# Performance work log

Measured on AMD Instinct MI355X. Metric: run time of the kernel, lower is better.

Reference implementation:

```python
import jax, jax.numpy as jnp
import numpy as np

B, N, C, H = 8, 4096, 1024, 16
D = C // H
SCALE = D ** -0.5

def setup_inputs() -> dict:
    key = jax.random.key(0)
    ks = jax.random.split(key, 6)
    s = C ** -0.5
    return {
        "fea": jax.random.normal(ks[0], (B, N, C), jnp.float32),
        "embedding": jax.random.normal(ks[1], (B, 1, C), jnp.float32),
        "Wq": jax.random.normal(ks[2], (C, C), jnp.float32) * s,
        "Wk": jax.random.normal(ks[3], (C, C), jnp.float32) * s,
        "Wv": jax.random.normal(ks[4], (C, C), jnp.float32) * s,
        "Wp": jax.random.normal(ks[5], (C, C), jnp.float32) * s,
        "bp": jnp.zeros((C,), jnp.float32),
    }

def reference(fea, embedding, Wq, Wk, Wv, Wp, bp):
    # q: [B,N,H,D]; k,v: [B,H,D] (kv seq len is 1)
    q = (fea @ Wq.T).reshape(B, N, H, D)
    k = (embedding @ Wk.T).reshape(B, H, D)
    v = (embedding @ Wv.T).reshape(B, H, D)
    # attn scores [B,N,H]: single-token key -> per-head dot product
    attn = jax.nn.sigmoid(jnp.einsum("bnhd,bhd->bnh", q, k) * SCALE)
    # broadcast-weight v over sequence: [B,N,H,D] -> [B,N,C]
    feat = (attn[..., None] * v[:, None, :, :]).reshape(B, N, C)
    feat = feat @ Wp.T + bp
    return feat + fea
```

## Files before the change

kernel.cpp:

```cpp
#include <hip/hip_runtime.h>
#include <hip/hip_bf16.h>
#include <stdint.h>

#define B 8
#define N 4096
#define C 1024
#define H 16
#define D 64

static __device__ __forceinline__ float bf_lo(uint32_t u) {
    union { uint32_t i; float f; } c; c.i = u << 16; return c.f;
}
static __device__ __forceinline__ float bf_hi(uint32_t u) {
    union { uint32_t i; float f; } c; c.i = u & 0xffff0000u; return c.f;
}

__global__ __launch_bounds__(256, 2)
void kv_kernel(const float* __restrict__ emb,
               const float* __restrict__ Wk,
               const float* __restrict__ Wv,
               float* __restrict__ kbuf,
               float* __restrict__ vbuf) {
    int wave = (blockIdx.x * blockDim.x + threadIdx.x) >> 6;
    int lane = threadIdx.x & 63;
    int r = wave;
    const float* Wrow = (r < C) ? (Wk + (size_t)r * C) : (Wv + (size_t)(r - C) * C);
    float4 w4[4];
#pragma unroll
    for (int j = 0; j < 4; ++j) w4[j] = *(const float4*)(Wrow + (lane + 64 * j) * 4);
    float acc[B];
#pragma unroll
    for (int b = 0; b < B; ++b) {
        const float* e = emb + (size_t)b * C;
        float a = 0.f;
#pragma unroll
        for (int j = 0; j < 4; ++j) {
            float4 e4 = *(const float4*)(e + (lane + 64 * j) * 4);
            a += w4[j].x * e4.x + w4[j].y * e4.y + w4[j].z * e4.z + w4[j].w * e4.w;
        }
        acc[b] = a;
    }
#pragma unroll
    for (int off = 32; off; off >>= 1)
#pragma unroll
        for (int b = 0; b < B; ++b) acc[b] += __shfl_xor(acc[b], off, 64);
    if (lane == 0) {
        float* dst = (r < C) ? (kbuf + r) : (vbuf + (r - C));
#pragma unroll
        for (int b = 0; b < B; ++b) dst[b * C] = acc[b];
    }
}

__global__ __launch_bounds__(256, 2)
void wu_kernel(const float* __restrict__ Wq,
               const float* __restrict__ Wp,
               const float* __restrict__ kbuf,
               const float* __restrict__ vbuf,
               __hip_bfloat16* __restrict__ wbuf,
               __hip_bfloat16* __restrict__ ubuf) {
    int id = blockIdx.x;
    int which = id & 1; id >>= 1;
    int h = id % H;
    int b = id / H;
    int t = threadIdx.x;
    if (which == 0) {
        const float* kk = kbuf + (size_t)(b * H + h) * D;
        int c = t * 4;
        float4 acc = {0.f, 0.f, 0.f, 0.f};
#pragma unroll 8
        for (int d = 0; d < D; ++d) {
            float kvs = kk[d];
            float4 w4 = *(const float4*)(Wq + (size_t)(h * D + d) * C + c);
            acc.x += kvs * w4.x; acc.y += kvs * w4.y;
            acc.z += kvs * w4.z; acc.w += kvs * w4.w;
        }
        __hip_bfloat16* o = wbuf + (size_t)(b * H + h) * C + c;
        o[0] = __float2bfloat16(acc.x); o[1] = __float2bfloat16(acc.y);
        o[2] = __float2bfloat16(acc.z); o[3] = __float2bfloat16(acc.w);
    } else {
        const int q = t & 3;
        const float* vv = vbuf + (size_t)(b * H + h) * D + q * 16;
        float4 v4[4];
#pragma unroll
        for (int m = 0; m < 4; ++m) v4[m] = *(const float4*)(vv + m * 4);
#pragma unroll
        for (int p = 0; p < 16; ++p) {
            int cp = p * 64 + (t >> 2);
            const float* wp = Wp + (size_t)cp * C + h * D + q * 16;
            float acc = 0.f;
#pragma unroll
            for (int m = 0; m < 4; ++m) {
                float4 w4 = *(const float4*)(wp + m * 4);
                acc += w4.x * v4[m].x + w4.y * v4[m].y
                     + w4.z * v4[m].z + w4.w * v4[m].w;
            }
            acc += __shfl_xor(acc, 1, 64);
            acc += __shfl_xor(acc, 2, 64);
            if (q == 0) ubuf[(size_t)(b * H + h) * C + cp] = __float2bfloat16(acc);
        }
    }
}

__global__ __launch_bounds__(256, 2)
void main_kernel(const float* __restrict__ fea,
                 const __hip_bfloat16* __restrict__ wbuf,
                 const __hip_bfloat16* __restrict__ ubuf,
                 const float* __restrict__ bp,
                 float* __restrict__ out) {
    __shared__ uint32_t w_s[H * C / 2];
    __shared__ uint32_t u_s[H * C / 2];
    const int b = blockIdx.y;
    const int tile = blockIdx.x;
    const int tid = threadIdx.x;

    {
        const uint4* wsrc = (const uint4*)(wbuf + (size_t)b * H * C);
        const uint4* usrc = (const uint4*)(ubuf + (size_t)b * H * C);
        uint4* wdst = (uint4*)w_s;
        uint4* udst = (uint4*)u_s;
#pragma unroll
        for (int i = 0; i < H * C / 8 / 256; ++i) {
            wdst[tid + i * 256] = wsrc[tid + i * 256];
            udst[tid + i * 256] = usrc[tid + i * 256];
        }
    }
    __syncthreads();

    const int lane = tid & 63;
    const int wv = tid >> 6;
    const int row0 = tile * 64 + wv * 16;

    float4 bp4[4];
#pragma unroll
    for (int j = 0; j < 4; ++j) bp4[j] = *(const float4*)(bp + 4 * lane + 256 * j);

#pragma unroll 1
    for (int i = 0; i < 16; ++i) {
        const float* fr = fea + ((size_t)b * N + row0 + i) * C + 4 * lane;
        float4 f[4];
#pragma unroll
        for (int j = 0; j < 4; ++j) f[j] = *(const float4*)(fr + 256 * j);

        float4 acc[4];
#pragma unroll
        for (int j = 0; j < 4; ++j) {
            acc[j].x = f[j].x + bp4[j].x; acc[j].y = f[j].y + bp4[j].y;
            acc[j].z = f[j].z + bp4[j].z; acc[j].w = f[j].w + bp4[j].w;
        }

#pragma unroll 1
        for (int h = 0; h < H; ++h) {
            const uint32_t* wrow = w_s + h * (C / 2) + 2 * lane;
            float s = 0.f;
#pragma unroll
            for (int j = 0; j < 4; ++j) {
                uint2 p = *(const uint2*)(wrow + 128 * j);
                s += f[j].x * bf_lo(p.x) + f[j].y * bf_hi(p.x)
                   + f[j].z * bf_lo(p.y) + f[j].w * bf_hi(p.y);
            }
#pragma unroll
            for (int off = 32; off; off >>= 1) s += __shfl_xor(s, off, 64);
            float sig = 1.f / (1.f + __expf(-0.125f * s));

            const uint32_t* urow = u_s + h * (C / 2) + 2 * lane;
#pragma unroll
            for (int j = 0; j < 4; ++j) {
                uint2 p = *(const uint2*)(urow + 128 * j);
                acc[j].x += sig * bf_lo(p.x); acc[j].y += sig * bf_hi(p.x);
                acc[j].z += sig * bf_lo(p.y); acc[j].w += sig * bf_hi(p.y);
            }
        }

        float* op = out + ((size_t)b * N + row0 + i) * C + 4 * lane;
#pragma unroll
        for (int j = 0; j < 4; ++j) *(float4*)(op + 256 * j) = acc[j];
    }
}

extern "C" void kernel_launch(void* const* d_in, const int* in_sizes, int n_in,
                              void* d_out, int out_size, void* d_ws, size_t ws_size,
                              hipStream_t stream) {
    const float* fea = (const float*)d_in[0];
    const float* emb = (const float*)d_in[1];
    const float* Wq  = (const float*)d_in[2];
    const float* Wk  = (const float*)d_in[3];
    const float* Wv  = (const float*)d_in[4];
    const float* Wp  = (const float*)d_in[5];
    const float* bp  = (const float*)d_in[6];
    float* out = (float*)d_out;

    char* ws = (char*)d_ws;
    float* kbuf = (float*)ws;
    float* vbuf = (float*)(ws + 32 * 1024);
    __hip_bfloat16* wbuf = (__hip_bfloat16*)(ws + 64 * 1024);
    __hip_bfloat16* ubuf = (__hip_bfloat16*)(ws + 320 * 1024);

    hipLaunchKernelGGL(kv_kernel, dim3(2 * C / 4), dim3(256), 0, stream,
                       emb, Wk, Wv, kbuf, vbuf);
    hipLaunchKernelGGL(wu_kernel, dim3(B * H * 2), dim3(256), 0, stream,
                       Wq, Wp, kbuf, vbuf, wbuf, ubuf);
    hipLaunchKernelGGL(main_kernel, dim3(N / 64, B), dim3(256), 0, stream,
                       fea, wbuf, ubuf, bp, out);
}
```

Baseline: 321.1 us.

## Process two rows per wave, prefetch fea, use fp32 LDS tables, batch wu over B

The main kernel now uses 512-thread blocks of 128 rows and processes two rows per iteration, so each LDS load of the w/u tables is reused across both rows. The next row pair of fea is prefetched into registers while the current pair is computed. The bf16 tables are unpacked to fp32 once when staged into shared memory, which removes the per-use unpacking. wu_kernel now batches all 8 batch entries per thread so Wq and Wp are read once instead of once per batch, at the cost of 128KB LDS per block and higher register pressure that may lower occupancy.

```diff
diff --git a/kernel.cpp b/kernel.cpp
--- a/kernel.cpp
+++ b/kernel.cpp
@@ -51,7 +51,7 @@
     }
 }
 
-__global__ __launch_bounds__(256, 2)
+__global__ __launch_bounds__(256)
 void wu_kernel(const float* __restrict__ Wq,
                const float* __restrict__ Wp,
                const float* __restrict__ kbuf,
@@ -59,121 +59,162 @@
                __hip_bfloat16* __restrict__ wbuf,
                __hip_bfloat16* __restrict__ ubuf) {
     int id = blockIdx.x;
-    int which = id & 1; id >>= 1;
-    int h = id % H;
-    int b = id / H;
     int t = threadIdx.x;
-    if (which == 0) {
-        const float* kk = kbuf + (size_t)(b * H + h) * D;
-        int c = t * 4;
-        float4 acc = {0.f, 0.f, 0.f, 0.f};
-#pragma unroll 8
+    if (id < 64) {
+        int h = id >> 2;
+        int c = ((id & 3) << 8) + t;
+        const float* kk = kbuf + h * D;
+        float acc[B];
+#pragma unroll
+        for (int b = 0; b < B; ++b) acc[b] = 0.f;
+#pragma unroll 4
         for (int d = 0; d < D; ++d) {
-            float kvs = kk[d];
-            float4 w4 = *(const float4*)(Wq + (size_t)(h * D + d) * C + c);
-            acc.x += kvs * w4.x; acc.y += kvs * w4.y;
-            acc.z += kvs * w4.z; acc.w += kvs * w4.w;
-        }
-        __hip_bfloat16* o = wbuf + (size_t)(b * H + h) * C + c;
-        o[0] = __float2bfloat16(acc.x); o[1] = __float2bfloat16(acc.y);
-        o[2] = __float2bfloat16(acc.z); o[3] = __float2bfloat16(acc.w);
+            float wv = Wq[(size_t)(h * D + d) * C + c];
+#pragma unroll
+            for (int b = 0; b < B; ++b) acc[b] += kk[(size_t)b * C + d] * wv;
+        }
+#pragma unroll
+        for (int b = 0; b < B; ++b)
+            wbuf[(size_t)(b * H + h) * C + c] = __float2bfloat16(acc[b]);
     } else {
-        const int q = t & 3;
-        const float* vv = vbuf + (size_t)(b * H + h) * D + q * 16;
-        float4 v4[4];
-#pragma unroll
-        for (int m = 0; m < 4; ++m) v4[m] = *(const float4*)(vv + m * 4);
-#pragma unroll
-        for (int p = 0; p < 16; ++p) {
-            int cp = p * 64 + (t >> 2);
-            const float* wp = Wp + (size_t)cp * C + h * D + q * 16;
-            float acc = 0.f;
+        int id2 = id - 64;
+        int h = id2 >> 2;
+        int cp = ((id2 & 3) << 8) + t;
+        const float* vv = vbuf + h * D;
+        float aq[4][B];
+#pragma unroll
+        for (int q = 0; q < 4; ++q)
+#pragma unroll
+            for (int b = 0; b < B; ++b) aq[q][b] = 0.f;
+#pragma unroll
+        for (int q = 0; q < 4; ++q) {
 #pragma unroll
             for (int m = 0; m < 4; ++m) {
-                float4 w4 = *(const float4*)(wp + m * 4);
-                acc += w4.x * v4[m].x + w4.y * v4[m].y
-                     + w4.z * v4[m].z + w4.w * v4[m].w;
-            }
-            acc += __shfl_xor(acc, 1, 64);
-            acc += __shfl_xor(acc, 2, 64);
-            if (q == 0) ubuf[(size_t)(b * H + h) * C + cp] = __float2bfloat16(acc);
-        }
-    }
-}
-
-__global__ __launch_bounds__(256, 2)
+                int d0 = q * 16 + m * 4;
+                float4 w4 = *(const float4*)(Wp + (size_t)cp * C + h * D + d0);
+#pragma unroll
+                for (int b = 0; b < B; ++b) {
+                    const float* vb = vv + (size_t)b * C + d0;
+                    aq[q][b] += w4.x * vb[0] + w4.y * vb[1]
+                              + w4.z * vb[2] + w4.w * vb[3];
+                }
+            }
+        }
+#pragma unroll
+        for (int b = 0; b < B; ++b)
+            ubuf[(size_t)(b * H + h) * C + cp] =
+                __float2bfloat16((aq[0][b] + aq[1][b]) + (aq[2][b] + aq[3][b]));
+    }
+}
+
+__global__ __launch_bounds__(512)
 void main_kernel(const float* __restrict__ fea,
                  const __hip_bfloat16* __restrict__ wbuf,
                  const __hip_bfloat16* __restrict__ ubuf,
                  const float* __restrict__ bp,
                  float* __restrict__ out) {
-    __shared__ uint32_t w_s[H * C / 2];
-    __shared__ uint32_t u_s[H * C / 2];
+    __shared__ float w_f[H * C];
+    __shared__ float u_f[H * C];
     const int b = blockIdx.y;
     const int tile = blockIdx.x;
     const int tid = threadIdx.x;
 
     {
-        const uint4* wsrc = (const uint4*)(wbuf + (size_t)b * H * C);
-        const uint4* usrc = (const uint4*)(ubuf + (size_t)b * H * C);
-        uint4* wdst = (uint4*)w_s;
-        uint4* udst = (uint4*)u_s;
-#pragma unroll
-        for (int i = 0; i < H * C / 8 / 256; ++i) {
-            wdst[tid + i * 256] = wsrc[tid + i * 256];
-            udst[tid + i * 256] = usrc[tid + i * 256];
+        const uint32_t* wsrc = (const uint32_t*)(wbuf + (size_t)b * H * C);
+        const uint32_t* usrc = (const uint32_t*)(ubuf + (size_t)b * H * C);
+#pragma unroll
+        for (int i = 0; i < H * C / 2 / 512; ++i) {
+            int wi = tid + i * 512;
+            uint32_t pw = wsrc[wi];
+            uint32_t pu = usrc[wi];
+            *(float2*)(w_f + 2 * wi) = make_float2(bf_lo(pw), bf_hi(pw));
+            *(float2*)(u_f + 2 * wi) = make_float2(bf_lo(pu), bf_hi(pu));
         }
     }
     __syncthreads();
 
     const int lane = tid & 63;
     const int wv = tid >> 6;
-    const int row0 = tile * 64 + wv * 16;
+    const int row0 = tile * 128 + wv * 16;
 
     float4 bp4[4];
 #pragma unroll
     for (int j = 0; j < 4; ++j) bp4[j] = *(const float4*)(bp + 4 * lane + 256 * j);
 
+    const float* fbase = fea + ((size_t)b * N + row0) * C + 4 * lane;
+    float* obase = out + ((size_t)b * N + row0) * C + 4 * lane;
+
+    float4 fa[2][4];
+#pragma unroll
+    for (int r = 0; r < 2; ++r)
+#pragma unroll
+        for (int j = 0; j < 4; ++j)
+            fa[r][j] = *(const float4*)(fbase + (size_t)r * C + 256 * j);
+
 #pragma unroll 1
-    for (int i = 0; i < 16; ++i) {
-        const float* fr = fea + ((size_t)b * N + row0 + i) * C + 4 * lane;
-        float4 f[4];
-#pragma unroll
-        for (int j = 0; j < 4; ++j) f[j] = *(const float4*)(fr + 256 * j);
-
-        float4 acc[4];
-#pragma unroll
-        for (int j = 0; j < 4; ++j) {
-            acc[j].x = f[j].x + bp4[j].x; acc[j].y = f[j].y + bp4[j].y;
-            acc[j].z = f[j].z + bp4[j].z; acc[j].w = f[j].w + bp4[j].w;
-        }
+    for (int g = 0; g < 8; ++g) {
+        const int gp = (g < 7) ? g + 1 : g;
+        float4 fb[2][4];
+#pragma unroll
+        for (int r = 0; r < 2; ++r)
+#pragma unroll
+            for (int j = 0; j < 4; ++j)
+                fb[r][j] = *(const float4*)(fbase + (size_t)(2 * gp + r) * C + 256 * j);
+
+        float4 acc[2][4];
+#pragma unroll
+        for (int r = 0; r < 2; ++r)
+#pragma unroll
+            for (int j = 0; j < 4; ++j) {
+                acc[r][j].x = fa[r][j].x + bp4[j].x;
+                acc[r][j].y = fa[r][j].y + bp4[j].y;
+                acc[r][j].z = fa[r][j].z + bp4[j].z;
+                acc[r][j].w = fa[r][j].w + bp4[j].w;
+            }
 
 #pragma unroll 1
         for (int h = 0; h < H; ++h) {
-            const uint32_t* wrow = w_s + h * (C / 2) + 2 * lane;
-            float s = 0.f;
+            const float* wrow = w_f + h * C + 4 * lane;
+            float s[2];
+            s[0] = 0.f; s[1] = 0.f;
 #pragma unroll
             for (int j = 0; j < 4; ++j) {
-                uint2 p = *(const uint2*)(wrow + 128 * j);
-                s += f[j].x * bf_lo(p.x) + f[j].y * bf_hi(p.x)
-                   + f[j].z * bf_lo(p.y) + f[j].w * bf_hi(p.y);
-            }
-#pragma unroll
-            for (int off = 32; off; off >>= 1) s += __shfl_xor(s, off, 64);
-            float sig = 1.f / (1.f + __expf(-0.125f * s));
-
-            const uint32_t* urow = u_s + h * (C / 2) + 2 * lane;
+                float4 w4 = *(const float4*)(wrow + 256 * j);
+#pragma unroll
+                for (int r = 0; r < 2; ++r)
+                    s[r] += fa[r][j].x * w4.x + fa[r][j].y * w4.y
+                          + fa[r][j].z * w4.z + fa[r][j].w * w4.w;
+            }
+#pragma unroll
+            for (int off = 32; off; off >>= 1)
+#pragma unroll
+                for (int r = 0; r < 2; ++r) s[r] += __shfl_xor(s[r], off, 64);
+#pragma unroll
+            for (int r = 0; r < 2; ++r)
+                s[r] = 1.f / (1.f + __expf(-0.125f * s[r]));
+
+            const float* urow = u_f + h * C + 4 * lane;
 #pragma unroll
             for (int j = 0; j < 4; ++j) {
-                uint2 p = *(const uint2*)(urow + 128 * j);
-                acc[j].x += sig * bf_lo(p.x); acc[j].y += sig * bf_hi(p.x);
-                acc[j].z += sig * bf_lo(p.y); acc[j].w += sig * bf_hi(p.y);
-            }
-        }
-
-        float* op = out + ((size_t)b * N + row0 + i) * C + 4 * lane;
-#pragma unroll
-        for (int j = 0; j < 4; ++j) *(float4*)(op + 256 * j) = acc[j];
+                float4 u4 = *(const float4*)(urow + 256 * j);
+#pragma unroll
+                for (int r = 0; r < 2; ++r) {
+                    acc[r][j].x += s[r] * u4.x; acc[r][j].y += s[r] * u4.y;
+                    acc[r][j].z += s[r] * u4.z; acc[r][j].w += s[r] * u4.w;
+                }
+            }
+        }
+
+#pragma unroll
+        for (int r = 0; r < 2; ++r)
+#pragma unroll
+            for (int j = 0; j < 4; ++j)
+                *(float4*)(obase + (size_t)(2 * g + r) * C + 256 * j) = acc[r][j];
+
+#pragma unroll
+        for (int r = 0; r < 2; ++r)
+#pragma unroll
+            for (int j = 0; j < 4; ++j) fa[r][j] = fb[r][j];
     }
 }
 
@@ -197,8 +238,8 @@
 
     hipLaunchKernelGGL(kv_kernel, dim3(2 * C / 4), dim3(256), 0, stream,
                        emb, Wk, Wv, kbuf, vbuf);
-    hipLaunchKernelGGL(wu_kernel, dim3(B * H * 2), dim3(256), 0, stream,
+    hipLaunchKernelGGL(wu_kernel, dim3(128), dim3(256), 0, stream,
                        Wq, Wp, kbuf, vbuf, wbuf, ubuf);
-    hipLaunchKernelGGL(main_kernel, dim3(N / 64, B), dim3(256), 0, stream,
+    hipLaunchKernelGGL(main_kernel, dim3(N / 128, B), dim3(512), 0, stream,
                        fea, wbuf, ubuf, bp, out);
 }
```

After: 291.0 us. 9.4% less time.
